# Optimization experiments

Measured on AMD Instinct MI355X. Metric: run time of the kernel, lower is better.

The kernel has to match this reference:

```python
import jax, jax.numpy as jnp
import numpy as np

GRID_SIZE = 5
SPLINE_ORDER = 3
GRID_RANGE = (-1.0, 1.0)
NUM_COEF = GRID_SIZE + SPLINE_ORDER  # 8


def make_grid(in_features):
    h = (GRID_RANGE[1] - GRID_RANGE[0]) / GRID_SIZE
    g = jnp.arange(-SPLINE_ORDER, GRID_SIZE + SPLINE_ORDER + 1, dtype=jnp.float32) * h + GRID_RANGE[0]
    return jnp.broadcast_to(g, (in_features, g.shape[0]))  # (in, grid_size + 2*order + 1)


def b_splines(x, grid):
    # x: (N, in); grid: (in, G). Cox-de Boor recursion -> (N, in, grid_size+order)
    xe = x[..., None]
    bases = ((xe >= grid[:, :-1]) & (xe < grid[:, 1:])).astype(x.dtype)
    for k in range(1, SPLINE_ORDER + 1):
        left = (xe - grid[:, : -(k + 1)]) / (grid[:, k:-1] - grid[:, : -(k + 1)])
        right = (grid[:, k + 1:] - xe) / (grid[:, k + 1:] - grid[:, 1:-k])
        bases = left * bases[..., :-1] + right * bases[..., 1:]
    return bases


def kan_linear(x, grid, base_w, spline_w, scaler):
    # base path: silu(x) @ base_w.T   (base_w: (out, in))
    base_out = jnp.einsum('ni,oi->no', jax.nn.silu(x), base_w)
    # spline path: flatten basis and scaled spline weights into one GEMM
    basis = b_splines(x, grid)                       # (N, in, 8)
    sw = spline_w * scaler[..., None]                # (out, in, 8)
    spline_out = jnp.einsum('nik,oik->no', basis, sw)
    return base_out + spline_out


def setup_inputs() -> dict:
    key = jax.random.key(0)
    ks = jax.random.split(key, 8)
    d = 1024
    dff = 4 * d
    n_tok = 4096
    s = 0.02
    return {
        'x': jax.random.normal(ks[0], (n_tok, d), dtype=jnp.float32),
        'base_w1': jax.random.normal(ks[1], (dff, d), dtype=jnp.float32) * s,
        'spline_w1': jax.random.normal(ks[2], (dff, d, NUM_COEF), dtype=jnp.float32) * s,
        'scaler1': jnp.ones((dff, d), dtype=jnp.float32),
        'base_w2': jax.random.normal(ks[3], (d, dff), dtype=jnp.float32) * s,
        'spline_w2': jax.random.normal(ks[4], (d, dff, NUM_COEF), dtype=jnp.float32) * s,
        'scaler2': jnp.ones((d, dff), dtype=jnp.float32),
        'grid1': make_grid(d),
        'grid2': make_grid(dff),
    }


def reference(x, base_w1, spline_w1, scaler1, base_w2, spline_w2, scaler2, grid1, grid2):
    h = kan_linear(x, grid1, base_w1, spline_w1, scaler1)
    h = jax.nn.gelu(h, approximate=False)  # torch nn.GELU default (erf)
    h = kan_linear(h, grid2, base_w2, spline_w2, scaler2)
    # Dropout(0.1) is identity in eval mode
    return h + x
```

## Files before the change

### kernel.cpp

```cpp
#include <hip/hip_runtime.h>
#include <hip/hip_fp16.h>

typedef _Float16 half_t;
typedef __attribute__((ext_vector_type(8))) _Float16 half8;
typedef __attribute__((ext_vector_type(4))) float f32x4;

#define AS1 __attribute__((address_space(1)))
#define AS3 __attribute__((address_space(3)))

__device__ __forceinline__ void gload16(const half_t* g, half_t* l) {
  __builtin_amdgcn_global_load_lds((const AS1 void*)g, (AS3 void*)l, 16, 0, 0);
}

__device__ __forceinline__ void bspline8u(float x, float out[8]) {
  float g[12];
#pragma unroll
  for (int j = 0; j < 12; ++j) g[j] = (float)(j - 3) * 0.4f - 1.0f;
  float b[11];
#pragma unroll
  for (int j = 0; j < 11; ++j)
    b[j] = (x >= g[j] && x < g[j + 1]) ? 1.0f : 0.0f;
#pragma unroll
  for (int k = 1; k <= 3; ++k) {
#pragma unroll
    for (int j = 0; j + k < 11; ++j) {
      float rl = 1.0f / (g[j + k] - g[j]);
      float rr = 1.0f / (g[j + k + 1] - g[j + 1]);
      b[j] = ((x - g[j]) * rl) * b[j] + ((g[j + k + 1] - x) * rr) * b[j + 1];
    }
  }
#pragma unroll
  for (int j = 0; j < 8; ++j) out[j] = b[j];
}

__global__ void wconv_kernel(const float* __restrict__ bw, const float* __restrict__ sw,
                             const float* __restrict__ sc, half_t* __restrict__ W,
                             int ibits, int ldw) {
  int idx = blockIdx.x * 256 + threadIdx.x;
  int o = idx >> ibits;
  int i = idx & ((1 << ibits) - 1);
  int c = i >> 10;
  int il = i & 1023;
  float b = bw[idx];
  float scv = sc[idx];
  const float4* svp = (const float4*)sw;
  float4 s0 = svp[(size_t)idx * 2];
  float4 s1 = svp[(size_t)idx * 2 + 1];
  half_t* wrow = W + (size_t)o * ldw + c * 9216;
  wrow[il] = (half_t)b;
  half8 hv;
  hv[0] = (half_t)(s0.x * scv); hv[1] = (half_t)(s0.y * scv);
  hv[2] = (half_t)(s0.z * scv); hv[3] = (half_t)(s0.w * scv);
  hv[4] = (half_t)(s1.x * scv); hv[5] = (half_t)(s1.y * scv);
  hv[6] = (half_t)(s1.z * scv); hv[7] = (half_t)(s1.w * scv);
  *(half8*)&wrow[1024 + il * 8] = hv;
}

template <typename ST>
__global__ void expand_kernel(const ST* __restrict__ src, half_t* __restrict__ dst,
                              int Isrc, int i0, int dsub, int kexp) {
  int idx = blockIdx.x * 256 + threadIdx.x;
  int n = idx >> 10;
  int il = idx & 1023;
  float v = (float)src[(size_t)n * Isrc + i0 + il];
  float bs[8];
  bspline8u(v, bs);
  half_t* drow = dst + (size_t)n * kexp + (size_t)dsub * 9216;
  drow[il] = (half_t)(v / (1.0f + expf(-v)));
  half8 hb;
#pragma unroll
  for (int k = 0; k < 8; ++k) hb[k] = (half_t)bs[k];
  *(half8*)&drow[1024 + il * 8] = hb;
}

#define STA(c, t, h)                                                          \
  {                                                                           \
    int r0_ = wid * 8 + (h) * 64;                                             \
    const half_t* g_ = Abase + (size_t)(r0_ + srow) * ldkA +                  \
                       (size_t)(t) * 64 + scol;                               \
    gload16(g_, &As[c][r0_ * 64]);                                            \
    gload16(g_ + (size_t)128 * ldkA, &As[c][(r0_ + 128) * 64]);               \
  }
#define STB(c, t, h)                                                          \
  {                                                                           \
    int r0_ = (wid >> 2) * 64 + (wid & 3) * 8 + (h) * 32;                     \
    const half_t* g_ = Bbase + (size_t)(r0_ + srow) * ldkB +                  \
                       (size_t)(t) * 64 + scol;                               \
    gload16(g_, &Bs[c][r0_ * 64]);                                            \
    gload16(g_ + (size_t)128 * ldkB, &Bs[c][(r0_ + 128) * 64]);               \
  }
#define LOADAF(c, mh)                                                         \
  _Pragma("unroll") for (int a = 0; a < 4; ++a) {                             \
    int row_ = wm * 128 + (mh) * 64 + a * 16 + (lane & 15);                   \
    _Pragma("unroll") for (int ks = 0; ks < 2; ++ks) {                        \
      int ch_ = (ks * 4 + (lane >> 4)) ^ (lane & 7);                          \
      af[a][ks] = *(const half8*)&As[c][row_ * 64 + ch_ * 8];                 \
    }                                                                         \
  }
#define LOADBF(c, nh, bfv)                                                    \
  _Pragma("unroll") for (int b = 0; b < 2; ++b) {                             \
    int row_ = wn * 64 + (nh) * 32 + b * 16 + (lane & 15);                    \
    _Pragma("unroll") for (int ks = 0; ks < 2; ++ks) {                        \
      int ch_ = (ks * 4 + (lane >> 4)) ^ (lane & 7);                          \
      bfv[b][ks] = *(const half8*)&Bs[c][row_ * 64 + ch_ * 8];                \
    }                                                                         \
  }
#define DOPHASE(W, mh, nh, bfv, LOADS, STAGE)                                 \
  do {                                                                        \
    LOADS                                                                     \
    STAGE                                                                     \
    asm volatile("s_waitcnt vmcnt(" #W ")" ::: "memory");                     \
    __builtin_amdgcn_s_barrier();                                             \
    __builtin_amdgcn_sched_barrier(0);                                        \
    __builtin_amdgcn_s_setprio(1);                                            \
    _Pragma("unroll") for (int ks = 0; ks < 2; ++ks)                          \
      _Pragma("unroll") for (int a = 0; a < 4; ++a)                           \
        _Pragma("unroll") for (int b = 0; b < 2; ++b)                         \
          acc[(mh) * 4 + a][(nh) * 2 + b] =                                   \
              __builtin_amdgcn_mfma_f32_16x16x32_f16(                         \
                  af[a][ks], bfv[b][ks], acc[(mh) * 4 + a][(nh) * 2 + b],     \
                  0, 0, 0);                                                   \
    __builtin_amdgcn_s_setprio(0);                                            \
    __builtin_amdgcn_s_barrier();                                             \
    __builtin_amdgcn_sched_barrier(0);                                        \
  } while (0)

template <int MODE>
__global__ __launch_bounds__(512, 2) void gemm8_kernel(
    const half_t* __restrict__ A, const half_t* __restrict__ B,
    int ldkA, int ldkB, int kzLen,
    float* __restrict__ Cout, half_t* __restrict__ Hout, int ldc) {
  __shared__ __align__(16) half_t As[2][256 * 64];
  __shared__ __align__(16) half_t Bs[2][256 * 64];

  const int tid = threadIdx.x;
  const int wid = tid >> 6;
  const int lane = tid & 63;
  const int wm = wid >> 2;
  const int wn = wid & 3;

  const half_t* Abase = A + (size_t)blockIdx.x * 256 * ldkA +
                        (size_t)blockIdx.z * kzLen;
  const half_t* Bbase = B + (size_t)blockIdx.y * 256 * ldkB +
                        (size_t)blockIdx.z * kzLen;

  const int srow = lane >> 3;
  const int scol = ((lane & 7) ^ srow) * 8;

  const int nt = kzLen >> 6;

  f32x4 acc[8][4] = {};
  half8 af[4][2], bA[2][2], bB[2][2];

  STA(0, 0, 0); STB(0, 0, 0); STB(0, 0, 1); STA(0, 0, 1);
  STA(1, 1, 0); STB(1, 1, 0);
  asm volatile("s_waitcnt vmcnt(0)" ::: "memory");
  __builtin_amdgcn_s_barrier();
  __builtin_amdgcn_sched_barrier(0);

  for (int i = 0; i < (nt >> 1) - 1; ++i) {
    const int t = 2 * i;
    DOPHASE(6, 0, 0, bA, { LOADAF(0, 0) LOADBF(0, 0, bA) }, { STB(1, t + 1, 1); });
    DOPHASE(6, 0, 1, bB, { LOADBF(0, 1, bB) },              { STA(1, t + 1, 1); });
    DOPHASE(6, 1, 1, bB, { LOADAF(0, 1) },                  { STA(0, t + 2, 0); });
    DOPHASE(6, 1, 0, bA, {},                                { STB(0, t + 2, 0); });
    DOPHASE(6, 0, 0, bA, { LOADAF(1, 0) LOADBF(1, 0, bA) }, { STB(0, t + 2, 1); });
    DOPHASE(6, 0, 1, bB, { LOADBF(1, 1, bB) },              { STA(0, t + 2, 1); });
    DOPHASE(6, 1, 1, bB, { LOADAF(1, 1) },                  { STA(1, t + 3, 0); });
    DOPHASE(6, 1, 0, bA, {},                                { STB(1, t + 3, 0); });
  }
  {
    const int t = nt - 2;
    DOPHASE(6, 0, 0, bA, { LOADAF(0, 0) LOADBF(0, 0, bA) }, { STB(1, t + 1, 1); });
    DOPHASE(6, 0, 1, bB, { LOADBF(0, 1, bB) },              { STA(1, t + 1, 1); });
    DOPHASE(6, 1, 1, bB, { LOADAF(0, 1) },                  {});
    DOPHASE(6, 1, 0, bA, {},                                {});
    DOPHASE(4, 0, 0, bA, { LOADAF(1, 0) LOADBF(1, 0, bA) }, {});
    DOPHASE(2, 0, 1, bB, { LOADBF(1, 1, bB) },              {});
    DOPHASE(0, 1, 1, bB, { LOADAF(1, 1) },                  {});
    DOPHASE(0, 1, 0, bA, {},                                {});
  }

  const int r_lo = (lane >> 4) << 2;
  const int col0 = (int)blockIdx.y * 256 + wn * 64 + (lane & 15);
  const int row00 = (int)blockIdx.x * 256 + wm * 128 + r_lo;
#pragma unroll
  for (int mf = 0; mf < 8; ++mf)
#pragma unroll
    for (int nf = 0; nf < 4; ++nf)
#pragma unroll
      for (int j = 0; j < 4; ++j) {
        float v = acc[mf][nf][j];
        size_t off = (size_t)(row00 + mf * 16 + j) * ldc + col0 + nf * 16;
        if constexpr (MODE == 0) {
          v = 0.5f * v * (1.0f + erff(v * 0.70710678118654752f));
          Hout[off] = (half_t)v;
        } else {
          atomicAdd(&Cout[off], v);
        }
      }
}

extern "C" void kernel_launch(void* const* d_in, const int* in_sizes, int n_in,
                              void* d_out, int out_size, void* d_ws, size_t ws_size,
                              hipStream_t stream) {
  const float* x   = (const float*)d_in[0];
  const float* bw1 = (const float*)d_in[1];
  const float* sw1 = (const float*)d_in[2];
  const float* sc1 = (const float*)d_in[3];
  const float* bw2 = (const float*)d_in[4];
  const float* sw2 = (const float*)d_in[5];
  const float* sc2 = (const float*)d_in[6];
  float* out = (float*)d_out;

  const int LDK1 = 9216 + 64;
  const int LDK2 = 36864 + 64;
  const int LDK2H = 18432 + 64;

  half_t* Wbuf = (half_t*)d_ws;
  const size_t W_HALVES  = (size_t)4096 * LDK1;
  const size_t AF_HALVES = (size_t)4096 * LDK2;
  const size_t A2_HALVES = (size_t)4096 * LDK2H;
  const size_t A1_HALVES = (size_t)4096 * LDK1;
  const size_t HH_HALVES = (size_t)4096 * 4096;
  int abuf_chunks = 1;
  if (ws_size >= (W_HALVES + AF_HALVES + HH_HALVES) * sizeof(half_t))
    abuf_chunks = 4;
  else if (ws_size >= (W_HALVES + A2_HALVES + HH_HALVES) * sizeof(half_t))
    abuf_chunks = 2;
  half_t* Abuf = Wbuf + W_HALVES;
  half_t* Hh   = Abuf + (abuf_chunks == 4 ? AF_HALVES
                         : abuf_chunks == 2 ? A2_HALVES : A1_HALVES);

  const int T = 256;
  const int NB = (4096 * 1024) / T;

  hipMemcpyAsync(out, x, (size_t)4096 * 1024 * sizeof(float),
                 hipMemcpyDeviceToDevice, stream);

  wconv_kernel<<<NB, T, 0, stream>>>(bw1, sw1, sc1, Wbuf, 10, LDK1);
  expand_kernel<float><<<NB, T, 0, stream>>>(x, Abuf, 1024, 0, 0, LDK1);
  gemm8_kernel<0><<<dim3(16, 16, 1), 512, 0, stream>>>(
      Abuf, Wbuf, LDK1, LDK1, 9216, nullptr, Hh, 4096);

  wconv_kernel<<<NB, T, 0, stream>>>(bw2, sw2, sc2, Wbuf, 12, LDK2);
  if (abuf_chunks == 4) {
    for (int c = 0; c < 4; ++c)
      expand_kernel<half_t><<<NB, T, 0, stream>>>(Hh, Abuf, 4096, c * 1024, c, LDK2);
    gemm8_kernel<4><<<dim3(16, 4, 4), 512, 0, stream>>>(
        Abuf, Wbuf, LDK2, LDK2, 9216, out, nullptr, 1024);
  } else if (abuf_chunks == 2) {
    for (int c = 0; c < 2; ++c) {
      expand_kernel<half_t><<<NB, T, 0, stream>>>(Hh, Abuf, 4096, c * 2048, 0, LDK2H);
      expand_kernel<half_t><<<NB, T, 0, stream>>>(Hh, Abuf, 4096, c * 2048 + 1024, 1, LDK2H);
      gemm8_kernel<4><<<dim3(16, 4, 4), 512, 0, stream>>>(
          Abuf, Wbuf + (size_t)c * 18432, LDK2H, LDK2, 4608, out, nullptr, 1024);
    }
  } else {
    for (int c = 0; c < 4; ++c) {
      expand_kernel<half_t><<<NB, T, 0, stream>>>(Hh, Abuf, 4096, c * 1024, 0, LDK1);
      gemm8_kernel<4><<<dim3(16, 4, 4), 512, 0, stream>>>(
          Abuf, Wbuf + (size_t)c * 9216, LDK1, LDK2, 2304, out, nullptr, 1024);
    }
  }
}
```

Baseline: 822.5 us.

## Double-buffer MFMA fragment registers, fuse residual copy and merge expand launches

The GEMM inner loop now loads the LDS fragments for the next phase into alternate register sets (afX/afY, bAX/bAY) while the current MFMAs run, instead of loading right before use. Launch bounds drop to 1 block per CU to make room for the extra registers. The residual copy of x into out is folded into the first expand kernel, and the four layer-2 expand launches become one. This aims to hide LDS read latency and cut launch and copy overhead, at the cost of occupancy and added register pressure.

```diff
diff --git a/kernel.cpp b/kernel.cpp
--- a/kernel.cpp
+++ b/kernel.cpp
@@ -58,7 +58,8 @@
 
 template <typename ST>
 __global__ void expand_kernel(const ST* __restrict__ src, half_t* __restrict__ dst,
-                              int Isrc, int i0, int dsub, int kexp) {
+                              int Isrc, int i0, int dsub, int kexp,
+                              float* __restrict__ xout) {
   int idx = blockIdx.x * 256 + threadIdx.x;
   int n = idx >> 10;
   int il = idx & 1023;
@@ -71,6 +72,25 @@
 #pragma unroll
   for (int k = 0; k < 8; ++k) hb[k] = (half_t)bs[k];
   *(half8*)&drow[1024 + il * 8] = hb;
+  if (xout) xout[(size_t)n * Isrc + il] = v;
+}
+
+__global__ void expand4_kernel(const half_t* __restrict__ src, half_t* __restrict__ dst,
+                               int ldk2) {
+  int idx = blockIdx.x * 256 + threadIdx.x;
+  int n = idx >> 12;
+  int il4 = idx & 4095;
+  int c = il4 >> 10;
+  int il = il4 & 1023;
+  float v = (float)src[(size_t)n * 4096 + il4];
+  float bs[8];
+  bspline8u(v, bs);
+  half_t* drow = dst + (size_t)n * ldk2 + (size_t)c * 9216;
+  drow[il] = (half_t)(v / (1.0f + expf(-v)));
+  half8 hb;
+#pragma unroll
+  for (int k = 0; k < 8; ++k) hb[k] = (half_t)bs[k];
+  *(half8*)&drow[1024 + il * 8] = hb;
 }
 
 #define STA(c, t, h)                                                          \
@@ -89,27 +109,32 @@
     gload16(g_, &Bs[c][r0_ * 64]);                                            \
     gload16(g_ + (size_t)128 * ldkB, &Bs[c][(r0_ + 128) * 64]);               \
   }
-#define LOADAF(c, mh)                                                         \
+#define LOADAF(dst, c, mh)                                                    \
   _Pragma("unroll") for (int a = 0; a < 4; ++a) {                             \
     int row_ = wm * 128 + (mh) * 64 + a * 16 + (lane & 15);                   \
     _Pragma("unroll") for (int ks = 0; ks < 2; ++ks) {                        \
       int ch_ = (ks * 4 + (lane >> 4)) ^ (lane & 7);                          \
-      af[a][ks] = *(const half8*)&As[c][row_ * 64 + ch_ * 8];                 \
+      dst[a][ks] = *(const half8*)&As[c][row_ * 64 + ch_ * 8];                \
     }                                                                         \
   }
-#define LOADBF(c, nh, bfv)                                                    \
+#define LOADBF(dst, c, nh)                                                    \
   _Pragma("unroll") for (int b = 0; b < 2; ++b) {                             \
     int row_ = wn * 64 + (nh) * 32 + b * 16 + (lane & 15);                    \
     _Pragma("unroll") for (int ks = 0; ks < 2; ++ks) {                        \
       int ch_ = (ks * 4 + (lane >> 4)) ^ (lane & 7);                          \
-      bfv[b][ks] = *(const half8*)&Bs[c][row_ * 64 + ch_ * 8];                \
+      dst[b][ks] = *(const half8*)&Bs[c][row_ * 64 + ch_ * 8];                \
     }                                                                         \
   }
-#define DOPHASE(W, mh, nh, bfv, LOADS, STAGE)                                 \
+#define VM6 asm volatile("s_waitcnt vmcnt(6)" ::: "memory");
+#define VM4 asm volatile("s_waitcnt vmcnt(4)" ::: "memory");
+#define VM2 asm volatile("s_waitcnt vmcnt(2)" ::: "memory");
+#define VM0 asm volatile("s_waitcnt vmcnt(0)" ::: "memory");
+#define NOVM
+#define DOPHASE(afv, bfv, mh, nh, LOADS, STAGE, WAIT)                         \
   do {                                                                        \
     LOADS                                                                     \
     STAGE                                                                     \
-    asm volatile("s_waitcnt vmcnt(" #W ")" ::: "memory");                     \
+    WAIT                                                                      \
     __builtin_amdgcn_s_barrier();                                             \
     __builtin_amdgcn_sched_barrier(0);                                        \
     __builtin_amdgcn_s_setprio(1);                                            \
@@ -118,7 +143,7 @@
         _Pragma("unroll") for (int b = 0; b < 2; ++b)                         \
           acc[(mh) * 4 + a][(nh) * 2 + b] =                                   \
               __builtin_amdgcn_mfma_f32_16x16x32_f16(                         \
-                  af[a][ks], bfv[b][ks], acc[(mh) * 4 + a][(nh) * 2 + b],     \
+                  afv[a][ks], bfv[b][ks], acc[(mh) * 4 + a][(nh) * 2 + b],    \
                   0, 0, 0);                                                   \
     __builtin_amdgcn_s_setprio(0);                                            \
     __builtin_amdgcn_s_barrier();                                             \
@@ -126,7 +151,7 @@
   } while (0)
 
 template <int MODE>
-__global__ __launch_bounds__(512, 2) void gemm8_kernel(
+__global__ __launch_bounds__(512, 1) void gemm8_kernel(
     const half_t* __restrict__ A, const half_t* __restrict__ B,
     int ldkA, int ldkB, int kzLen,
     float* __restrict__ Cout, half_t* __restrict__ Hout, int ldc) {
@@ -150,35 +175,37 @@
   const int nt = kzLen >> 6;
 
   f32x4 acc[8][4] = {};
-  half8 af[4][2], bA[2][2], bB[2][2];
+  half8 afX[4][2], afY[4][2], bAX[2][2], bAY[2][2], bBv[2][2];
 
   STA(0, 0, 0); STB(0, 0, 0); STB(0, 0, 1); STA(0, 0, 1);
   STA(1, 1, 0); STB(1, 1, 0);
   asm volatile("s_waitcnt vmcnt(0)" ::: "memory");
   __builtin_amdgcn_s_barrier();
   __builtin_amdgcn_sched_barrier(0);
+  LOADAF(afX, 0, 0)
+  LOADBF(bAX, 0, 0)
 
   for (int i = 0; i < (nt >> 1) - 1; ++i) {
     const int t = 2 * i;
-    DOPHASE(6, 0, 0, bA, { LOADAF(0, 0) LOADBF(0, 0, bA) }, { STB(1, t + 1, 1); });
-    DOPHASE(6, 0, 1, bB, { LOADBF(0, 1, bB) },              { STA(1, t + 1, 1); });
-    DOPHASE(6, 1, 1, bB, { LOADAF(0, 1) },                  { STA(0, t + 2, 0); });
-    DOPHASE(6, 1, 0, bA, {},                                { STB(0, t + 2, 0); });
-    DOPHASE(6, 0, 0, bA, { LOADAF(1, 0) LOADBF(1, 0, bA) }, { STB(0, t + 2, 1); });
-    DOPHASE(6, 0, 1, bB, { LOADBF(1, 1, bB) },              { STA(0, t + 2, 1); });
-    DOPHASE(6, 1, 1, bB, { LOADAF(1, 1) },                  { STA(1, t + 3, 0); });
-    DOPHASE(6, 1, 0, bA, {},                                { STB(1, t + 3, 0); });
+    DOPHASE(afX, bAX, 0, 0, { LOADBF(bBv, 0, 1) }, { STB(1, t + 1, 1); }, VM6);
+    DOPHASE(afX, bBv, 0, 1, { LOADAF(afY, 0, 1) }, { STA(1, t + 1, 1); }, VM6);
+    DOPHASE(afY, bBv, 1, 1, { LOADAF(afX, 1, 0) }, { STA(0, t + 2, 0); }, VM6);
+    DOPHASE(afY, bAX, 1, 0, { LOADBF(bAY, 1, 0) }, { STB(0, t + 2, 0); }, VM6);
+    DOPHASE(afX, bAY, 0, 0, { LOADBF(bBv, 1, 1) }, { STB(0, t + 2, 1); }, VM6);
+    DOPHASE(afX, bBv, 0, 1, { LOADAF(afY, 1, 1) }, { STA(0, t + 2, 1); }, VM6);
+    DOPHASE(afY, bBv, 1, 1, { LOADAF(afX, 0, 0) }, { STA(1, t + 3, 0); }, VM6);
+    DOPHASE(afY, bAY, 1, 0, { LOADBF(bAX, 0, 0) }, { STB(1, t + 3, 0); }, VM6);
   }
   {
     const int t = nt - 2;
-    DOPHASE(6, 0, 0, bA, { LOADAF(0, 0) LOADBF(0, 0, bA) }, { STB(1, t + 1, 1); });
-    DOPHASE(6, 0, 1, bB, { LOADBF(0, 1, bB) },              { STA(1, t + 1, 1); });
-    DOPHASE(6, 1, 1, bB, { LOADAF(0, 1) },                  {});
-    DOPHASE(6, 1, 0, bA, {},                                {});
-    DOPHASE(4, 0, 0, bA, { LOADAF(1, 0) LOADBF(1, 0, bA) }, {});
-    DOPHASE(2, 0, 1, bB, { LOADBF(1, 1, bB) },              {});
-    DOPHASE(0, 1, 1, bB, { LOADAF(1, 1) },                  {});
-    DOPHASE(0, 1, 0, bA, {},                                {});
+    DOPHASE(afX, bAX, 0, 0, { LOADBF(bBv, 0, 1) }, { STB(1, t + 1, 1); }, VM6);
+    DOPHASE(afX, bBv, 0, 1, { LOADAF(afY, 0, 1) }, { STA(1, t + 1, 1); }, VM6);
+    DOPHASE(afY, bBv, 1, 1, { LOADAF(afX, 1, 0) }, {},                   VM4);
+    DOPHASE(afY, bAX, 1, 0, { LOADBF(bAY, 1, 0) }, {},                   VM2);
+    DOPHASE(afX, bAY, 0, 0, { LOADBF(bBv, 1, 1) }, {},                   VM0);
+    DOPHASE(afX, bBv, 0, 1, { LOADAF(afY, 1, 1) }, {},                   NOVM);
+    DOPHASE(afY, bBv, 1, 1, {},                    {},                   NOVM);
+    DOPHASE(afY, bAY, 1, 0, {},                    {},                   NOVM);
   }
 
   const int r_lo = (lane >> 4) << 2;
@@ -235,30 +262,26 @@
   const int T = 256;
   const int NB = (4096 * 1024) / T;
 
-  hipMemcpyAsync(out, x, (size_t)4096 * 1024 * sizeof(float),
-                 hipMemcpyDeviceToDevice, stream);
-
   wconv_kernel<<<NB, T, 0, stream>>>(bw1, sw1, sc1, Wbuf, 10, LDK1);
-  expand_kernel<float><<<NB, T, 0, stream>>>(x, Abuf, 1024, 0, 0, LDK1);
+  expand_kernel<float><<<NB, T, 0, stream>>>(x, Abuf, 1024, 0, 0, LDK1, out);
   gemm8_kernel<0><<<dim3(16, 16, 1), 512, 0, stream>>>(
       Abuf, Wbuf, LDK1, LDK1, 9216, nullptr, Hh, 4096);
 
   wconv_kernel<<<NB, T, 0, stream>>>(bw2, sw2, sc2, Wbuf, 12, LDK2);
   if (abuf_chunks == 4) {
-    for (int c = 0; c < 4; ++c)
-      expand_kernel<half_t><<<NB, T, 0, stream>>>(Hh, Abuf, 4096, c * 1024, c, LDK2);
+    expand4_kernel<<<4 * NB, T, 0, stream>>>(Hh, Abuf, LDK2);
     gemm8_kernel<4><<<dim3(16, 4, 4), 512, 0, stream>>>(
         Abuf, Wbuf, LDK2, LDK2, 9216, out, nullptr, 1024);
   } else if (abuf_chunks == 2) {
     for (int c = 0; c < 2; ++c) {
-      expand_kernel<half_t><<<NB, T, 0, stream>>>(Hh, Abuf, 4096, c * 2048, 0, LDK2H);
-      expand_kernel<half_t><<<NB, T, 0, stream>>>(Hh, Abuf, 4096, c * 2048 + 1024, 1, LDK2H);
+      expand_kernel<half_t><<<NB, T, 0, stream>>>(Hh, Abuf, 4096, c * 2048, 0, LDK2H, nullptr);
+      expand_kernel<half_t><<<NB, T, 0, stream>>>(Hh, Abuf, 4096, c * 2048 + 1024, 1, LDK2H, nullptr);
       gemm8_kernel<4><<<dim3(16, 4, 4), 512, 0, stream>>>(
           Abuf, Wbuf + (size_t)c * 18432, LDK2H, LDK2, 4608, out, nullptr, 1024);
     }
   } else {
     for (int c = 0; c < 4; ++c) {
-      expand_kernel<half_t><<<NB, T, 0, stream>>>(Hh, Abuf, 4096, c * 1024, 0, LDK1);
+      expand_kernel<half_t><<<NB, T, 0, stream>>>(Hh, Abuf, 4096, c * 1024, 0, LDK1, nullptr);
       gemm8_kernel<4><<<dim3(16, 4, 4), 512, 0, stream>>>(
           Abuf, Wbuf + (size_t)c * 9216, LDK1, LDK2, 2304, out, nullptr, 1024);
     }
```

After: 1.680 ms. +104.3%, slower.

## Vectorize expand kernels, fuse residual copy, and regroup GEMM stage waits

Applied to the files above, without the earlier changes.

Replaces the scalar expand kernels with vectorized versions that process 4 or 8 elements per thread. The residual copy of x into out is folded into the first expand kernel, and the four per-chunk expand launches for layer two become one launch. In the GEMM main loop, two stage loads are merged into one phase and the vmcnt waits are raised so more global-to-LDS loads stay in flight. The new wait counts must still match the number of outstanding loads, or LDS data could be read before it arrives.

```diff
diff --git a/kernel.cpp b/kernel.cpp
--- a/kernel.cpp
+++ b/kernel.cpp
@@ -3,6 +3,7 @@
 
 typedef _Float16 half_t;
 typedef __attribute__((ext_vector_type(8))) _Float16 half8;
+typedef __attribute__((ext_vector_type(4))) _Float16 half4;
 typedef __attribute__((ext_vector_type(4))) float f32x4;
 
 #define AS1 __attribute__((address_space(1)))
@@ -56,6 +57,29 @@
   *(half8*)&wrow[1024 + il * 8] = hv;
 }
 
+__global__ void expand1v4_kernel(const float* __restrict__ x, half_t* __restrict__ dst,
+                                 int kexp, float* __restrict__ xout) {
+  int idx = blockIdx.x * 256 + threadIdx.x;
+  int n = idx >> 8;
+  int i4 = (idx & 255) * 4;
+  float4 v = *(const float4*)&x[(size_t)n * 1024 + i4];
+  half_t* drow = dst + (size_t)n * kexp;
+  float vv[4] = {v.x, v.y, v.z, v.w};
+  half4 bh;
+#pragma unroll
+  for (int j = 0; j < 4; ++j) {
+    float bs[8];
+    bspline8u(vv[j], bs);
+    bh[j] = (half_t)(vv[j] / (1.0f + expf(-vv[j])));
+    half8 hb;
+#pragma unroll
+    for (int k = 0; k < 8; ++k) hb[k] = (half_t)bs[k];
+    *(half8*)&drow[1024 + (i4 + j) * 8] = hb;
+  }
+  *(half4*)&drow[i4] = bh;
+  *(float4*)&xout[(size_t)n * 1024 + i4] = v;
+}
+
 template <typename ST>
 __global__ void expand_kernel(const ST* __restrict__ src, half_t* __restrict__ dst,
                               int Isrc, int i0, int dsub, int kexp) {
@@ -73,6 +97,30 @@
   *(half8*)&drow[1024 + il * 8] = hb;
 }
 
+__global__ void expand4v8_kernel(const half_t* __restrict__ src, half_t* __restrict__ dst,
+                                 int ldk2) {
+  int idx = blockIdx.x * 256 + threadIdx.x;
+  int n = idx >> 9;
+  int e8 = (idx & 511) * 8;
+  int c = e8 >> 10;
+  int il = e8 & 1023;
+  half8 hv = *(const half8*)&src[(size_t)n * 4096 + e8];
+  half_t* drow = dst + (size_t)n * ldk2 + (size_t)c * 9216;
+  half8 bh;
+#pragma unroll
+  for (int j = 0; j < 8; ++j) {
+    float v = (float)hv[j];
+    float bs[8];
+    bspline8u(v, bs);
+    bh[j] = (half_t)(v / (1.0f + expf(-v)));
+    half8 hb;
+#pragma unroll
+    for (int k = 0; k < 8; ++k) hb[k] = (half_t)bs[k];
+    *(half8*)&drow[1024 + (il + j) * 8] = hb;
+  }
+  *(half8*)&drow[il] = bh;
+}
+
 #define STA(c, t, h)                                                          \
   {                                                                           \
     int r0_ = wid * 8 + (h) * 64;                                             \
@@ -105,11 +153,16 @@
       bfv[b][ks] = *(const half8*)&Bs[c][row_ * 64 + ch_ * 8];                \
     }                                                                         \
   }
-#define DOPHASE(W, mh, nh, bfv, LOADS, STAGE)                                 \
+#define VM8 asm volatile("s_waitcnt vmcnt(8)" ::: "memory");
+#define VM4 asm volatile("s_waitcnt vmcnt(4)" ::: "memory");
+#define VM2 asm volatile("s_waitcnt vmcnt(2)" ::: "memory");
+#define VM0 asm volatile("s_waitcnt vmcnt(0)" ::: "memory");
+#define NOVM
+#define DOPHASE(mh, nh, bfv, LOADS, STAGE, WAIT)                              \
   do {                                                                        \
     LOADS                                                                     \
     STAGE                                                                     \
-    asm volatile("s_waitcnt vmcnt(" #W ")" ::: "memory");                     \
+    WAIT                                                                      \
     __builtin_amdgcn_s_barrier();                                             \
     __builtin_amdgcn_sched_barrier(0);                                        \
     __builtin_amdgcn_s_setprio(1);                                            \
@@ -160,25 +213,25 @@
 
   for (int i = 0; i < (nt >> 1) - 1; ++i) {
     const int t = 2 * i;
-    DOPHASE(6, 0, 0, bA, { LOADAF(0, 0) LOADBF(0, 0, bA) }, { STB(1, t + 1, 1); });
-    DOPHASE(6, 0, 1, bB, { LOADBF(0, 1, bB) },              { STA(1, t + 1, 1); });
-    DOPHASE(6, 1, 1, bB, { LOADAF(0, 1) },                  { STA(0, t + 2, 0); });
-    DOPHASE(6, 1, 0, bA, {},                                { STB(0, t + 2, 0); });
-    DOPHASE(6, 0, 0, bA, { LOADAF(1, 0) LOADBF(1, 0, bA) }, { STB(0, t + 2, 1); });
-    DOPHASE(6, 0, 1, bB, { LOADBF(1, 1, bB) },              { STA(0, t + 2, 1); });
-    DOPHASE(6, 1, 1, bB, { LOADAF(1, 1) },                  { STA(1, t + 3, 0); });
-    DOPHASE(6, 1, 0, bA, {},                                { STB(1, t + 3, 0); });
+    DOPHASE(0, 0, bA, { LOADAF(0, 0) LOADBF(0, 0, bA) }, { STB(1, t + 1, 1); }, VM8);
+    DOPHASE(0, 1, bB, { LOADBF(0, 1, bB) },              { STA(1, t + 1, 1); }, VM8);
+    DOPHASE(1, 1, bB, { LOADAF(0, 1) },                  { STA(0, t + 2, 0); }, VM8);
+    DOPHASE(1, 0, bA, {},                                { STB(0, t + 2, 0); }, VM8);
+    DOPHASE(0, 0, bA, { LOADAF(1, 0) LOADBF(1, 0, bA) }, { STB(0, t + 2, 1); }, VM8);
+    DOPHASE(0, 1, bB, { LOADBF(1, 1, bB) },              { STA(0, t + 2, 1); }, VM8);
+    DOPHASE(1, 1, bB, { LOADAF(1, 1) },                  { STA(1, t + 3, 0); STB(1, t + 3, 0); }, VM8);
+    DOPHASE(1, 0, bA, {},                                {},                    VM8);
   }
   {
     const int t = nt - 2;
-    DOPHASE(6, 0, 0, bA, { LOADAF(0, 0) LOADBF(0, 0, bA) }, { STB(1, t + 1, 1); });
-    DOPHASE(6, 0, 1, bB, { LOADBF(0, 1, bB) },              { STA(1, t + 1, 1); });
-    DOPHASE(6, 1, 1, bB, { LOADAF(0, 1) },                  {});
-    DOPHASE(6, 1, 0, bA, {},                                {});
-    DOPHASE(4, 0, 0, bA, { LOADAF(1, 0) LOADBF(1, 0, bA) }, {});
-    DOPHASE(2, 0, 1, bB, { LOADBF(1, 1, bB) },              {});
-    DOPHASE(0, 1, 1, bB, { LOADAF(1, 1) },                  {});
-    DOPHASE(0, 1, 0, bA, {},                                {});
+    DOPHASE(0, 0, bA, { LOADAF(0, 0) LOADBF(0, 0, bA) }, { STB(1, t + 1, 1); }, VM8);
+    DOPHASE(0, 1, bB, { LOADBF(0, 1, bB) },              { STA(1, t + 1, 1); }, VM8);
+    DOPHASE(1, 1, bB, { LOADAF(0, 1) },                  {},                    VM8);
+    DOPHASE(1, 0, bA, {},                                {},                    VM4);
+    DOPHASE(0, 0, bA, { LOADAF(1, 0) LOADBF(1, 0, bA) }, {},                    VM2);
+    DOPHASE(0, 1, bB, { LOADBF(1, 1, bB) },              {},                    VM0);
+    DOPHASE(1, 1, bB, { LOADAF(1, 1) },                  {},                    NOVM);
+    DOPHASE(1, 0, bA, {},                                {},                    NOVM);
   }
 
   const int r_lo = (lane >> 4) << 2;
@@ -235,18 +288,14 @@
   const int T = 256;
   const int NB = (4096 * 1024) / T;
 
-  hipMemcpyAsync(out, x, (size_t)4096 * 1024 * sizeof(float),
-                 hipMemcpyDeviceToDevice, stream);
-
   wconv_kernel<<<NB, T, 0, stream>>>(bw1, sw1, sc1, Wbuf, 10, LDK1);
-  expand_kernel<float><<<NB, T, 0, stream>>>(x, Abuf, 1024, 0, 0, LDK1);
+  expand1v4_kernel<<<NB / 4, T, 0, stream>>>(x, Abuf, LDK1, out);
   gemm8_kernel<0><<<dim3(16, 16, 1), 512, 0, stream>>>(
       Abuf, Wbuf, LDK1, LDK1, 9216, nullptr, Hh, 4096);
 
   wconv_kernel<<<NB, T, 0, stream>>>(bw2, sw2, sc2, Wbuf, 12, LDK2);
   if (abuf_chunks == 4) {
-    for (int c = 0; c < 4; ++c)
-      expand_kernel<half_t><<<NB, T, 0, stream>>>(Hh, Abuf, 4096, c * 1024, c, LDK2);
+    expand4v8_kernel<<<NB / 2, T, 0, stream>>>(Hh, Abuf, LDK2);
     gemm8_kernel<4><<<dim3(16, 4, 4), 512, 0, stream>>>(
         Abuf, Wbuf, LDK2, LDK2, 9216, out, nullptr, 1024);
   } else if (abuf_chunks == 2) {
```

After: 864.9 us. 5.2% more time.
